# Kernel optimization log

Hardware: AMD Instinct MI355X
Metric: run time of the kernel (lower is better)

## Reference

```python
import jax, jax.numpy as jnp
import numpy as np

B, S, D, E, H, K = 64, 2048, 1024, 32, 4096, 8


def setup_inputs() -> dict:
    key = jax.random.key(0)
    k0, k1, k2, k3 = jax.random.split(key, 4)
    x = jax.random.normal(k0, (B, S, D), jnp.float32)
    # gate: nn.Linear(D, E) -> weight [E, D], bias [E]
    gate_w = jax.random.normal(k1, (E, D), jnp.float32) * (1.0 / np.sqrt(D))
    gate_b = jnp.zeros((E,), jnp.float32)
    # expert weights include the bias row (input dim + 1)
    w1 = jax.random.normal(k2, (E, D + 1, H), jnp.float32) * (1.0 / np.sqrt(D + 1))
    w2 = jax.random.normal(k3, (E, H + 1, D), jnp.float32) * (1.0 / np.sqrt(H + 1))
    return {"x": x, "gate_w": gate_w, "gate_b": gate_b, "w1": w1, "w2": w2}


def reference(x, gate_w, gate_b, w1, w2):
    b, s, d = x.shape
    # gating: softmax over the TOKEN axis (expert-choice routing)
    logits = jnp.einsum('bsd,ed->bse', x, gate_w) + gate_b          # [b, s, E]
    probs = jax.nn.softmax(logits, axis=-2)                          # softmax over tokens
    # top-k tokens per expert (torch.topk over dim=-2)
    vals_t, idx_t = jax.lax.top_k(probs.transpose(0, 2, 1), K)      # [b, E, k]
    vals = vals_t.transpose(0, 2, 1)                                 # [b, k, E]
    idx = idx_t.transpose(0, 2, 1)                                   # [b, k, E]
    flat_idx = idx.reshape(b, K * E)                                 # gather order: [k, E] flattened
    # gather selected tokens
    tok = jnp.take_along_axis(x, flat_idx[:, :, None], axis=1)       # [b, k*E, d]
    tok = tok.reshape(b, K, E, d)
    # weighted merge (mux) of the k tokens per expert
    merged = jnp.einsum('bked,bke->bed', tok, vals)                  # [b, E, d]
    ones = jnp.ones(merged.shape[:-1] + (1,), merged.dtype)
    # expert FFN (bias folded into the extra weight row)
    h = jnp.einsum('bei,eih->beh', jnp.concatenate([merged, ones], -1), w1)
    h = jax.nn.gelu(h, approximate=False)                            # torch nn.GELU() = exact erf
    o = jnp.einsum('bej,ejo->beo', jnp.concatenate([h, ones], -1), w2)  # [b, E, d]
    # demux: broadcast expert output back to its k tokens, weighted, scatter-add
    out_tok = jnp.einsum('beo,bke->bkeo', o, vals).reshape(b, K * E, d)
    out = jnp.zeros_like(x).at[jnp.arange(b)[:, None], flat_idx].add(out_tok)
    return out
```

## Files before the change

kernel.cpp:

```cpp
#include <hip/hip_runtime.h>
#include <hip/hip_bf16.h>
#include <math.h>

constexpr int NB = 64;
constexpr int NS = 2048;
constexpr int ND = 1024;
constexpr int NE = 32;
constexpr int NH = 4096;
constexpr int NK = 8;

typedef short bf16x8 __attribute__((ext_vector_type(8)));
typedef float f32x4  __attribute__((ext_vector_type(4)));

__device__ __forceinline__ unsigned short f2bf_rne(float v) {
  unsigned u = __builtin_bit_cast(unsigned, v);
  u += 0x7fffu + ((u >> 16) & 1u);
  return (unsigned short)(u >> 16);
}

__device__ __forceinline__ void gload_lds16(const void* g, void* l) {
  __builtin_amdgcn_global_load_lds(
      (const __attribute__((address_space(1))) unsigned*)g,
      (__attribute__((address_space(3))) unsigned*)l, 16, 0, 0);
}

__device__ __forceinline__ unsigned ford(float f) {
  unsigned u = __builtin_bit_cast(unsigned, f);
  return (u & 0x80000000u) ? ~u : (u | 0x80000000u);
}
__device__ __forceinline__ float finv(unsigned o) {
  unsigned u = (o & 0x80000000u) ? (o & 0x7fffffffu) : ~o;
  return __builtin_bit_cast(float, u);
}

__global__ __launch_bounds__(256) void k_gate_mfma(const float* __restrict__ x,
                                                   const float* __restrict__ gw,
                                                   float* __restrict__ logitsT) {
  const int b  = blockIdx.y;
  const int s0 = blockIdx.x * 64;
  const int t  = threadIdx.x;
  const int l  = t & 63;
  const int w  = t >> 6;

  __shared__ char smem[24576];
  float* trans = (float*)smem;

  f32x4 acc[2] = {};

  const int ar  = t >> 2;
  const int ac4 = (t & 3) * 16;
  const int ge  = t >> 3;
  const int gk  = (t & 7) * 8;

  float xA[4][4], xB[4][4], wA[8], wB[8];

  auto issue = [&](int kt, float (&xreg)[4][4], float (&wreg)[8]) {
    const int k0 = kt * 64;
    const float* xr = &x[((size_t)b * NS + s0 + ar) * ND + k0 + ac4];
#pragma unroll
    for (int j = 0; j < 4; ++j) *(float4*)xreg[j] = *(const float4*)&xr[j * 4];
    *(float4*)&wreg[0] = *(const float4*)&gw[(size_t)ge * ND + k0 + gk];
    *(float4*)&wreg[4] = *(const float4*)&gw[(size_t)ge * ND + k0 + gk + 4];
  };
  auto commit = [&](int dst, float (&xreg)[4][4], float (&wreg)[8]) {
    short* Ah = (short*)(smem + dst * 8192);
    short* Bh = (short*)(smem + 16384 + dst * 4096);
#pragma unroll
    for (int j = 0; j < 4; ++j) {
      unsigned short h[4];
#pragma unroll
      for (int q = 0; q < 4; ++q) h[q] = f2bf_rne(xreg[j][q]);
      const int col = ac4 + j * 4;
      *(ushort4*)&Ah[ar * 64 + (col ^ ((ar & 7) * 8))] = *(const ushort4*)h;
    }
    unsigned short h8[8];
#pragma unroll
    for (int j = 0; j < 8; ++j) h8[j] = f2bf_rne(wreg[j]);
    *(uint4*)&Bh[ge * 64 + (gk ^ ((ge & 7) * 8))] = *(const uint4*)h8;
  };
  auto mfma_phase = [&](int cur) {
    const short* Ah = (const short*)(smem + cur * 8192);
    const short* Bh = (const short*)(smem + 16384 + cur * 4096);
#pragma unroll
    for (int ks = 0; ks < 2; ++ks) {
      const int koff = ks * 32 + (l >> 4) * 8;
      const int rl = w * 16 + (l & 15);
      bf16x8 a = *(const bf16x8*)&Ah[rl * 64 + (koff ^ ((rl & 7) * 8))];
#pragma unroll
      for (int nf = 0; nf < 2; ++nf) {
        const int n = nf * 16 + (l & 15);
        bf16x8 bb = *(const bf16x8*)&Bh[n * 64 + (koff ^ ((n & 7) * 8))];
        acc[nf] = __builtin_amdgcn_mfma_f32_16x16x32_bf16(a, bb, acc[nf], 0, 0, 0);
      }
    }
  };
  auto bar = [&]() {
    asm volatile("s_waitcnt lgkmcnt(0)" ::: "memory");
    __builtin_amdgcn_s_barrier();
    __builtin_amdgcn_sched_barrier(0);
  };

  issue(0, xA, wA);
  issue(1, xB, wB);
  commit(0, xA, wA);
  bar();

  for (int kt = 0; kt < ND / 64; kt += 2) {
    if (kt + 2 < ND / 64) issue(kt + 2, xA, wA);
    commit(1, xB, wB);
    mfma_phase(0);
    bar();
    if (kt + 3 < ND / 64) issue(kt + 3, xB, wB);
    if (kt + 2 < ND / 64) commit(0, xA, wA);
    mfma_phase(1);
    bar();
  }

#pragma unroll
  for (int nf = 0; nf < 2; ++nf)
#pragma unroll
    for (int j = 0; j < 4; ++j) {
      const int sl = w * 16 + (l >> 4) * 4 + j;
      const int ec = nf * 16 + (l & 15);
      trans[sl * 33 + ec] = acc[nf][j];
    }
  __syncthreads();
  const int eo = t >> 3, sc = (t & 7) * 8;
#pragma unroll
  for (int q = 0; q < 2; ++q) {
    float4 v;
    v.x = trans[(sc + q * 4 + 0) * 33 + eo];
    v.y = trans[(sc + q * 4 + 1) * 33 + eo];
    v.z = trans[(sc + q * 4 + 2) * 33 + eo];
    v.w = trans[(sc + q * 4 + 3) * 33 + eo];
    *(float4*)&logitsT[((size_t)b * NE + eo) * NS + s0 + sc + q * 4] = v;
  }
}

__global__ __launch_bounds__(256) void k_topk_merge(const float* __restrict__ logitsT,
                                                    const float* __restrict__ x,
                                                    const float* __restrict__ gw,
                                                    float* __restrict__ tval,
                                                    int* __restrict__ tidx,
                                                    unsigned short* __restrict__ A1) {
  const int be = blockIdx.x, b = be >> 5, e = be & 31;
  const float* row = logitsT + (size_t)be * NS;
  const int t = threadIdx.x, w = t >> 6, lane = t & 63;

  __shared__ unsigned long long cvp[64];
  __shared__ int    gci[16];
  __shared__ float  glc[16];
  __shared__ double wsum[4];
  __shared__ float  smax_s;
  __shared__ double ginv;
  __shared__ float  selv[8];
  __shared__ int    seli[8];

  float v[8]; int si[8];
#pragma unroll
  for (int j = 0; j < 8; ++j) {
    const int s = w * 512 + lane + j * 64;
    v[j] = row[s]; si[j] = s;
  }
#pragma unroll
  for (int i = 0; i < 7; ++i)
#pragma unroll
    for (int j = 0; j < 7 - i; ++j) {
      const bool sw = (v[j + 1] > v[j]) || (v[j + 1] == v[j] && si[j + 1] < si[j]);
      const float tv = sw ? v[j + 1] : v[j];
      const int   ti = sw ? si[j + 1] : si[j];
      v[j + 1] = sw ? v[j] : v[j + 1];  si[j + 1] = sw ? si[j] : si[j + 1];
      v[j] = tv;  si[j] = ti;
    }
  const float mxl = v[0];
  double s8 = 1.0;
#pragma unroll
  for (int j = 1; j < 8; ++j) s8 += (double)expf(v[j] - mxl);

  unsigned long long p[8];
#pragma unroll
  for (int j = 0; j < 8; ++j)
    p[j] = ((unsigned long long)ford(v[j]) << 32) | (0xFFFFFFFFu - (unsigned)si[j]);

  for (int r = 0; r < 16; ++r) {
    unsigned long long m = p[0];
#pragma unroll
    for (int off = 1; off < 64; off <<= 1) {
      const unsigned long long o = __shfl_xor(m, off);
      m = (o > m) ? o : m;
    }
    if (lane == 0) cvp[w * 16 + r] = m;
    if (p[0] == m) {
      p[0]=p[1]; p[1]=p[2]; p[2]=p[3]; p[3]=p[4]; p[4]=p[5]; p[5]=p[6]; p[6]=p[7]; p[7]=0ull;
    }
  }
  __syncthreads();

  if (w == 0) {
    const unsigned long long mine = cvp[lane];
    int rank = 0;
#pragma unroll
    for (int j = 0; j < 64; ++j) rank += (cvp[j] > mine);
    if (rank < 16) {
      gci[rank] = (int)(0xFFFFFFFFu - (unsigned)(mine & 0xFFFFFFFFu));
      if (rank == 0) smax_s = finv((unsigned)(mine >> 32));
    }
  }
  __syncthreads();

  const float mx = smax_s;
  double lsum = s8 * (double)expf(mxl - mx);
#pragma unroll
  for (int off = 32; off; off >>= 1) lsum += __shfl_xor(lsum, off);
  if (lane == 0) wsum[w] = lsum;
  __syncthreads();
  if (t == 0) ginv = 1.0 / (wsum[0] + wsum[1] + wsum[2] + wsum[3]);

  const int kb = lane * 16;
  float gwl[16];
  *(float4*)&gwl[0]  = *(const float4*)&gw[(size_t)e * ND + kb];
  *(float4*)&gwl[4]  = *(const float4*)&gw[(size_t)e * ND + kb + 4];
  *(float4*)&gwl[8]  = *(const float4*)&gw[(size_t)e * ND + kb + 8];
  *(float4*)&gwl[12] = *(const float4*)&gw[(size_t)e * ND + kb + 12];
#pragma unroll
  for (int q = 0; q < 4; ++q) {
    const int c = w * 4 + q;
    const int ciq = gci[c];
    const float* xr = x + ((size_t)b * NS + ciq) * ND + kb;
    float xv[16];
    *(float4*)&xv[0]  = *(const float4*)&xr[0];
    *(float4*)&xv[4]  = *(const float4*)&xr[4];
    *(float4*)&xv[8]  = *(const float4*)&xr[8];
    *(float4*)&xv[12] = *(const float4*)&xr[12];
    double d = 0.0;
#pragma unroll
    for (int j2 = 0; j2 < 16; ++j2) d += (double)xv[j2] * (double)gwl[j2];
#pragma unroll
    for (int off = 32; off; off >>= 1) d += __shfl_xor(d, off);
    if (lane == 0) glc[c] = (float)d;
  }
  __syncthreads();
  if (t < 16) {
    const float mylc = glc[t]; const int myci = gci[t];
    int rank = 0;
#pragma unroll
    for (int c2 = 0; c2 < 16; ++c2) {
      if (c2 == t) continue;
      rank += (glc[c2] > mylc) || (glc[c2] == mylc && gci[c2] < myci);
    }
    if (rank < 8) {
      const float pv = (float)((double)expf(mylc - mx) * ginv);
      tval[be * 8 + rank] = pv;
      tidx[be * 8 + rank] = myci;
      selv[rank] = pv;
      seli[rank] = myci;
    }
  }
  __syncthreads();

  float4 acc4 = {0.f, 0.f, 0.f, 0.f};
#pragma unroll
  for (int k = 0; k < 8; ++k) {
    const float vv = selv[k];
    const int   ss = seli[k];
    const float4 xv4 = *(const float4*)&x[((size_t)b * NS + ss) * ND + t * 4];
    acc4.x += vv * xv4.x; acc4.y += vv * xv4.y;
    acc4.z += vv * xv4.z; acc4.w += vv * xv4.w;
  }
  const int kt = t >> 4;
  const int g  = (t & 15) >> 1;
  const size_t off = ((size_t)(e * 16 + kt)) * 4096 + b * 64 + ((g ^ (b & 7)) << 3) + (t & 1) * 4;
  unsigned short h4[4] = {f2bf_rne(acc4.x), f2bf_rne(acc4.y), f2bf_rne(acc4.z), f2bf_rne(acc4.w)};
  *(ushort4*)&A1[off] = *(const ushort4*)h4;
}

template <int K, int N, bool GELU>
__global__ __launch_bounds__(256, 4) void k_ffn(const unsigned short* __restrict__ AT,
                                                const float* __restrict__ W,
                                                unsigned short* __restrict__ OT,
                                                float* __restrict__ Of) {
  constexpr int KT = K / 64;
  const int e  = blockIdx.y;
  const int n0 = blockIdx.x * 64;
  const int t  = threadIdx.x, l = t & 63, w = t >> 6;
  const int wr = w >> 1, wc = w & 1;

  __shared__ char smem[32768];

  const float* Wbase = W + (size_t)e * (K + 1) * N;
  f32x4 acc[2][2] = {};

  const int wn  = l;
  const int wk0 = w * 8;
  float wreg[2][8];

  auto issueW = [&](int kt) {
    const float* Wg = Wbase + (size_t)(kt * 64) * N + n0 + wn;
#pragma unroll
    for (int rn = 0; rn < 2; ++rn)
#pragma unroll
      for (int j = 0; j < 8; ++j)
        wreg[rn][j] = Wg[(size_t)(wk0 + rn * 32 + j) * N];
  };
  auto issueA = [&](int kt, int dst) {
    const unsigned short* at = AT + ((size_t)(e * KT + kt)) * 4096;
    char* Ab = smem + dst * 8192;
#pragma unroll
    for (int p = 0; p < 2; ++p)
      gload_lds16(at + p * 2048 + t * 8, Ab + p * 4096 + w * 1024);
  };
  auto commitW = [&](int dst) {
    short* Bb = (short*)(smem + 16384 + dst * 8192);
#pragma unroll
    for (int rn = 0; rn < 2; ++rn) {
      const int kr = (wk0 + rn * 32) >> 3;
      unsigned short s8[8];
#pragma unroll
      for (int j = 0; j < 8; ++j) s8[j] = f2bf_rne(wreg[rn][j]);
      *(uint4*)&Bb[wn * 64 + ((kr ^ (wn & 7)) << 3)] = *(const uint4*)s8;
    }
  };
  auto mfma_phase = [&](int cur) {
    const short* Ab = (const short*)(smem + cur * 8192);
    const short* Bb = (const short*)(smem + 16384 + cur * 8192);
#pragma unroll
    for (int ks = 0; ks < 2; ++ks) {
      const int g8 = ks * 4 + (l >> 4);
      bf16x8 a[2], bb[2];
#pragma unroll
      for (int mf = 0; mf < 2; ++mf) {
        const int m = wr * 32 + mf * 16 + (l & 15);
        a[mf] = *(const bf16x8*)&Ab[m * 64 + ((g8 ^ (m & 7)) << 3)];
      }
#pragma unroll
      for (int nf = 0; nf < 2; ++nf) {
        const int n = wc * 32 + nf * 16 + (l & 15);
        bb[nf] = *(const bf16x8*)&Bb[n * 64 + ((g8 ^ (n & 7)) << 3)];
      }
#pragma unroll
      for (int mf = 0; mf < 2; ++mf)
#pragma unroll
        for (int nf = 0; nf < 2; ++nf)
          acc[mf][nf] = __builtin_amdgcn_mfma_f32_16x16x32_bf16(a[mf], bb[nf], acc[mf][nf], 0, 0, 0);
    }
  };

  issueW(0); issueA(0, 0);
  commitW(0);
  __syncthreads();
  int cur = 0;
  for (int kt = 0; kt < KT; ++kt) {
    const bool more = (kt + 1 < KT);
    if (more) { issueW(kt + 1); issueA(kt + 1, cur ^ 1); }
    mfma_phase(cur);
    if (more) commitW(cur ^ 1);
    __syncthreads();
    cur ^= 1;
  }

  if (GELU) {
    unsigned short* transU = (unsigned short*)smem;
#pragma unroll
    for (int nf = 0; nf < 2; ++nf) {
      const int c = wc * 32 + nf * 16 + (l & 15);
      const float bias = Wbase[(size_t)K * N + n0 + c];
#pragma unroll
      for (int mf = 0; mf < 2; ++mf)
#pragma unroll
        for (int j = 0; j < 4; ++j) {
          const int m = wr * 32 + mf * 16 + (l >> 4) * 4 + j;
          float vv = acc[mf][nf][j] + bias;
          vv = 0.5f * vv * (1.0f + erff(vv * 0.70710678118654752440f));
          transU[m * 72 + c] = f2bf_rne(vv);
        }
    }
    __syncthreads();
    const int m  = t >> 2;
    const int c0 = (t & 3) * 16;
    const size_t tb = ((size_t)(e * (N / 64) + blockIdx.x)) * 4096;
    uint4 v0 = *(const uint4*)&transU[m * 72 + c0];
    uint4 v1 = *(const uint4*)&transU[m * 72 + c0 + 8];
    const int g0 = c0 >> 3;
    *(uint4*)&OT[tb + m * 64 + ((g0 ^ (m & 7)) << 3)]       = v0;
    *(uint4*)&OT[tb + m * 64 + (((g0 + 1) ^ (m & 7)) << 3)] = v1;
  } else {
    float* transF = (float*)smem;
#pragma unroll
    for (int nf = 0; nf < 2; ++nf) {
      const int c = wc * 32 + nf * 16 + (l & 15);
      const float bias = Wbase[(size_t)K * N + n0 + c];
#pragma unroll
      for (int mf = 0; mf < 2; ++mf)
#pragma unroll
        for (int j = 0; j < 4; ++j) {
          const int m = wr * 32 + mf * 16 + (l >> 4) * 4 + j;
          transF[m * 68 + c] = acc[mf][nf][j] + bias;
        }
    }
    __syncthreads();
    const int m  = t >> 2;
    const int c0 = (t & 3) * 16;
    float* og = Of + ((size_t)m * NE + e) * ND + n0 + c0;
    *(float4*)&og[0]  = *(const float4*)&transF[m * 68 + c0];
    *(float4*)&og[4]  = *(const float4*)&transF[m * 68 + c0 + 4];
    *(float4*)&og[8]  = *(const float4*)&transF[m * 68 + c0 + 8];
    *(float4*)&og[12] = *(const float4*)&transF[m * 68 + c0 + 12];
  }
}

__global__ __launch_bounds__(256) void k_scatter(const float* __restrict__ Obuf,
                                                 const float* __restrict__ tval,
                                                 const int* __restrict__ tidx,
                                                 float* __restrict__ out) {
  const int s0 = blockIdx.x * 8;
  const int b  = blockIdx.y;
  const int t  = threadIdx.x;
  const int w  = t >> 6;
  __shared__ unsigned long long masks[8][4];

  const int myIdx = tidx[b * 256 + t];
#pragma unroll
  for (int j = 0; j < 8; ++j) {
    unsigned long long m = __ballot(myIdx == s0 + j);
    if ((t & 63) == 0) masks[j][w] = m;
  }
  __syncthreads();

#pragma unroll
  for (int j = 0; j < 8; ++j) {
    float4 acc = {0.f, 0.f, 0.f, 0.f};
#pragma unroll
    for (int q = 0; q < 4; ++q) {
      unsigned long long mm = masks[j][q];
      while (mm) {
        int bit = __ffsll(mm) - 1;
        mm &= mm - 1;
        int r = q * 64 + bit;
        float v = tval[b * 256 + r];
        const float4 ov = *(const float4*)&Obuf[((size_t)b * NE + (r >> 3)) * ND + t * 4];
        acc.x += v * ov.x; acc.y += v * ov.y; acc.z += v * ov.z; acc.w += v * ov.w;
      }
    }
    *(float4*)&out[((size_t)b * NS + s0 + j) * ND + t * 4] = acc;
  }
}

extern "C" void kernel_launch(void* const* d_in, const int* in_sizes, int n_in,
                              void* d_out, int out_size, void* d_ws, size_t ws_size,
                              hipStream_t stream) {
  const float* x  = (const float*)d_in[0];
  const float* gw = (const float*)d_in[1];
  const float* w1 = (const float*)d_in[3];
  const float* w2 = (const float*)d_in[4];
  float* out = (float*)d_out;

  char* ws = (char*)d_ws;
  float* logitsT     = (float*)ws;
  float* tval        = (float*)(ws + 16777216);
  int*   tidx        = (int*)  (ws + 16842752);
  unsigned short* A1 = (unsigned short*)(ws + 16908288);
  unsigned short* Hb = (unsigned short*)(ws + 21102592);
  float* Obuf        = (float*)(ws + 37879808);

  k_gate_mfma<<<dim3(NS / 64, NB), 256, 0, stream>>>(x, gw, logitsT);
  k_topk_merge<<<NB * NE, 256, 0, stream>>>(logitsT, x, gw, tval, tidx, A1);
  k_ffn<ND, NH, true ><<<dim3(NH / 64, NE), 256, 0, stream>>>(A1, w1, Hb, nullptr);
  k_ffn<NH, ND, false><<<dim3(ND / 64, NE), 256, 0, stream>>>(Hb, w2, nullptr, Obuf);
  k_scatter<<<dim3(NS / 8, NB), 256, 0, stream>>>(Obuf, tval, tidx, out);
}
```

Before: 506.7 us.

## Load gate GEMM operands directly into MFMA registers, dropping LDS staging

The gating GEMM kernel used to stage x and gate weights through double-buffered LDS, with a barrier between phases. Now each lane loads its own MFMA fragment straight from global memory into registers and converts it to bf16 there, double-buffering in registers, with no LDS staging and no barriers. The intent is to remove LDS traffic and synchronisation. In exchange, each wave loads the gate weights redundantly, and the per-lane 32-byte row-strided loads of x may coalesce less well.

```diff
diff --git a/kernel.cpp b/kernel.cpp
--- a/kernel.cpp
+++ b/kernel.cpp
@@ -16,6 +16,12 @@
   unsigned u = __builtin_bit_cast(unsigned, v);
   u += 0x7fffu + ((u >> 16) & 1u);
   return (unsigned short)(u >> 16);
+}
+__device__ __forceinline__ bf16x8 cvt8(const float (&f)[8]) {
+  unsigned short h[8];
+#pragma unroll
+  for (int j = 0; j < 8; ++j) h[j] = f2bf_rne(f[j]);
+  return *(const bf16x8*)h;
 }
 
 __device__ __forceinline__ void gload_lds16(const void* g, void* l) {
@@ -42,78 +48,49 @@
   const int l  = t & 63;
   const int w  = t >> 6;
 
-  __shared__ char smem[24576];
-  float* trans = (float*)smem;
+  __shared__ float trans[64 * 33];
 
   f32x4 acc[2] = {};
 
-  const int ar  = t >> 2;
-  const int ac4 = (t & 3) * 16;
-  const int ge  = t >> 3;
-  const int gk  = (t & 7) * 8;
-
-  float xA[4][4], xB[4][4], wA[8], wB[8];
-
-  auto issue = [&](int kt, float (&xreg)[4][4], float (&wreg)[8]) {
+  const int klane = (l >> 4) * 8;
+  const float* xrow = x  + ((size_t)b * NS + s0 + w * 16 + (l & 15)) * ND + klane;
+  const float* g0   = gw + (size_t)(l & 15) * ND + klane;
+  const float* g1   = gw + (size_t)(16 + (l & 15)) * ND + klane;
+
+  float aA[2][8], b0A[2][8], b1A[2][8];
+  float aB[2][8], b0B[2][8], b1B[2][8];
+
+  auto loadT = [&](int kt, float (&a)[2][8], float (&b0)[2][8], float (&b1)[2][8]) {
     const int k0 = kt * 64;
-    const float* xr = &x[((size_t)b * NS + s0 + ar) * ND + k0 + ac4];
-#pragma unroll
-    for (int j = 0; j < 4; ++j) *(float4*)xreg[j] = *(const float4*)&xr[j * 4];
-    *(float4*)&wreg[0] = *(const float4*)&gw[(size_t)ge * ND + k0 + gk];
-    *(float4*)&wreg[4] = *(const float4*)&gw[(size_t)ge * ND + k0 + gk + 4];
-  };
-  auto commit = [&](int dst, float (&xreg)[4][4], float (&wreg)[8]) {
-    short* Ah = (short*)(smem + dst * 8192);
-    short* Bh = (short*)(smem + 16384 + dst * 4096);
-#pragma unroll
-    for (int j = 0; j < 4; ++j) {
-      unsigned short h[4];
-#pragma unroll
-      for (int q = 0; q < 4; ++q) h[q] = f2bf_rne(xreg[j][q]);
-      const int col = ac4 + j * 4;
-      *(ushort4*)&Ah[ar * 64 + (col ^ ((ar & 7) * 8))] = *(const ushort4*)h;
-    }
-    unsigned short h8[8];
-#pragma unroll
-    for (int j = 0; j < 8; ++j) h8[j] = f2bf_rne(wreg[j]);
-    *(uint4*)&Bh[ge * 64 + (gk ^ ((ge & 7) * 8))] = *(const uint4*)h8;
-  };
-  auto mfma_phase = [&](int cur) {
-    const short* Ah = (const short*)(smem + cur * 8192);
-    const short* Bh = (const short*)(smem + 16384 + cur * 4096);
 #pragma unroll
     for (int ks = 0; ks < 2; ++ks) {
-      const int koff = ks * 32 + (l >> 4) * 8;
-      const int rl = w * 16 + (l & 15);
-      bf16x8 a = *(const bf16x8*)&Ah[rl * 64 + (koff ^ ((rl & 7) * 8))];
-#pragma unroll
-      for (int nf = 0; nf < 2; ++nf) {
-        const int n = nf * 16 + (l & 15);
-        bf16x8 bb = *(const bf16x8*)&Bh[n * 64 + (koff ^ ((n & 7) * 8))];
-        acc[nf] = __builtin_amdgcn_mfma_f32_16x16x32_bf16(a, bb, acc[nf], 0, 0, 0);
-      }
-    }
-  };
-  auto bar = [&]() {
-    asm volatile("s_waitcnt lgkmcnt(0)" ::: "memory");
-    __builtin_amdgcn_s_barrier();
-    __builtin_amdgcn_sched_barrier(0);
-  };
-
-  issue(0, xA, wA);
-  issue(1, xB, wB);
-  commit(0, xA, wA);
-  bar();
-
+      const int kk = k0 + ks * 32;
+      *(float4*)&a[ks][0]  = *(const float4*)&xrow[kk];
+      *(float4*)&a[ks][4]  = *(const float4*)&xrow[kk + 4];
+      *(float4*)&b0[ks][0] = *(const float4*)&g0[kk];
+      *(float4*)&b0[ks][4] = *(const float4*)&g0[kk + 4];
+      *(float4*)&b1[ks][0] = *(const float4*)&g1[kk];
+      *(float4*)&b1[ks][4] = *(const float4*)&g1[kk + 4];
+    }
+  };
+  auto mfmaT = [&](float (&a)[2][8], float (&b0)[2][8], float (&b1)[2][8]) {
+#pragma unroll
+    for (int ks = 0; ks < 2; ++ks) {
+      const bf16x8 av  = cvt8(a[ks]);
+      const bf16x8 b0v = cvt8(b0[ks]);
+      const bf16x8 b1v = cvt8(b1[ks]);
+      acc[0] = __builtin_amdgcn_mfma_f32_16x16x32_bf16(av, b0v, acc[0], 0, 0, 0);
+      acc[1] = __builtin_amdgcn_mfma_f32_16x16x32_bf16(av, b1v, acc[1], 0, 0, 0);
+    }
+  };
+
+  loadT(0, aA, b0A, b1A);
+  loadT(1, aB, b0B, b1B);
   for (int kt = 0; kt < ND / 64; kt += 2) {
-    if (kt + 2 < ND / 64) issue(kt + 2, xA, wA);
-    commit(1, xB, wB);
-    mfma_phase(0);
-    bar();
-    if (kt + 3 < ND / 64) issue(kt + 3, xB, wB);
-    if (kt + 2 < ND / 64) commit(0, xA, wA);
-    mfma_phase(1);
-    bar();
+    mfmaT(aA, b0A, b1A);
+    if (kt + 2 < ND / 64) loadT(kt + 2, aA, b0A, b1A);
+    mfmaT(aB, b0B, b1B);
+    if (kt + 3 < ND / 64) loadT(kt + 3, aB, b0B, b1B);
   }
 
 #pragma unroll
```

After: 540.6 us. +6.7%, slower.
